# Optimization experiments

Hardware: AMD Instinct MI355X
Metric: run time of the kernel (lower is better)

## Reference

```python
import jax, jax.numpy as jnp
import numpy as np

NUM_EXECUTORS = 50
NUM_DAG_FEATURES = 3
EMB_DAG = 16
EMB_GLOB = 16
HIDDEN = [64, 64, 32]
B = 60000            # number of jobs (one per env in the batched rollout)
NODES_PER_JOB = 10
NODE_FEAT = 5


def _init_mlp(key, dims):
    ws, bs = [], []
    for i in range(len(dims) - 1):
        key, k = jax.random.split(key)
        scale = 1.0 / np.sqrt(dims[i])
        ws.append(jax.random.uniform(k, (dims[i], dims[i + 1]), jnp.float32, -scale, scale))
        bs.append(jnp.zeros((dims[i + 1],), jnp.float32))
    return ws, bs


def setup_inputs() -> dict:
    rng = np.random.default_rng(0)
    n_nodes = B * NODES_PER_JOB
    # dag_batch.ptr: job i owns nodes [i*NODES_PER_JOB, (i+1)*NODES_PER_JOB)
    ptr = np.arange(B + 1, dtype=np.int64) * NODES_PER_JOB
    job_indices = rng.permutation(B).astype(np.int64)
    # ragged action counts per job (exec_mask is a prefix mask of length num_exec_acts[i])
    num_exec_acts = rng.integers(1, NUM_EXECUTORS + 1, size=B).astype(np.int64)
    n_sel = num_exec_acts[job_indices]
    T = int(n_sel.sum())
    # per-ragged-row executor index: concat([arange(n) for n in n_sel]), vectorized
    starts = np.cumsum(n_sel) - n_sel
    exec_act_idx = (np.arange(T, dtype=np.int64) - np.repeat(starts, n_sel)).astype(np.int64)

    key = jax.random.key(0)
    k_x, k_hd, k_hg, k_mlp = jax.random.split(key, 4)
    x = jax.random.normal(k_x, (n_nodes, NODE_FEAT), jnp.float32)
    h_dag = jax.random.normal(k_hd, (B, EMB_DAG), jnp.float32)
    h_glob = jax.random.normal(k_hg, (B, EMB_GLOB), jnp.float32)

    in_dim = NUM_DAG_FEATURES + EMB_DAG + EMB_GLOB + 1  # 36
    ws, bs = _init_mlp(k_mlp, [in_dim] + HIDDEN + [1])

    return {
        "x": x,
        "h_dag": h_dag,
        "h_glob": h_glob,
        "ptr": jnp.asarray(ptr),
        "job_indices": jnp.asarray(job_indices),
        "num_exec_acts": jnp.asarray(num_exec_acts),
        "exec_act_idx": jnp.asarray(exec_act_idx),
        "W1": ws[0], "b1": bs[0],
        "W2": ws[1], "b2": bs[1],
        "W3": ws[2], "b3": bs[2],
        "W4": ws[3], "b4": bs[3],
    }


def reference(x, h_dag, h_glob, ptr, job_indices, num_exec_acts, exec_act_idx,
              W1, b1, W2, b2, W3, b3, W4, b4):
    T = exec_act_idx.shape[0]                       # total ragged action rows (static)
    J = job_indices.shape[0]
    # masked gather: dag features at each dag's start node, then select jobs
    x_dag = x[ptr[:-1], :NUM_DAG_FEATURES][job_indices]        # [J, 3]
    h_dag_sel = h_dag[job_indices]                              # [J, 16]
    x_h_dag = jnp.concatenate([x_dag, h_dag_sel], axis=1)       # [J, 19]
    # variable repeat_interleave -> gather by repeated row index
    n_sel = num_exec_acts[job_indices]
    rpt = jnp.repeat(jnp.arange(J), n_sel, total_repeat_length=T)
    x_h_rpt = x_h_dag[rpt]                                      # [T, 19]
    h_glob_rpt = h_glob[rpt]                                    # [T, 16]
    # exec action feature: k / num_executors for the k-th valid executor
    exec_actions = (exec_act_idx.astype(x.dtype) / NUM_EXECUTORS)[:, None]  # [T, 1]
    h = jnp.concatenate([x_h_rpt, h_glob_rpt, exec_actions], axis=1)        # [T, 36]
    h = jax.nn.relu(h @ W1 + b1)
    h = jax.nn.relu(h @ W2 + b2)
    h = jax.nn.relu(h @ W3 + b3)
    scores = (h @ W4 + b4).squeeze(-1)                          # [T]
    return scores
```

## Files before the change

kernel.cpp:

```cpp
#include <hip/hip_runtime.h>

#define TPB 256

using half8  = __attribute__((ext_vector_type(8))) _Float16;
using fp16x2 = __attribute__((ext_vector_type(2))) __fp16;
using f32x4  = __attribute__((ext_vector_type(4))) float;

static __device__ __forceinline__ unsigned short h2u(_Float16 h) {
    union { _Float16 h; unsigned short u; } v; v.h = h; return v.u;
}
static __device__ __forceinline__ unsigned pkrtz(float a, float b) {
    fp16x2 h = __builtin_amdgcn_cvt_pkrtz(a, b);
    return __builtin_bit_cast(unsigned, h);
}
template <int CTRL>
static __device__ __forceinline__ float dppmov(float x) {
    return __int_as_float(__builtin_amdgcn_mov_dpp(__float_as_int(x), CTRL, 0xF, 0xF, true));
}
#define DPP_SWAP 0xB1

__global__ __launch_bounds__(TPB) void k_prep(const float* __restrict__ x,
                                              const float* __restrict__ h_dag,
                                              const float* __restrict__ h_glob,
                                              const int* __restrict__ ptr,
                                              const int* __restrict__ job_indices,
                                              const int* __restrict__ num_exec_acts,
                                              int J, unsigned int* __restrict__ feat,
                                              int* __restrict__ bsum, int* __restrict__ jsv)
{
    __shared__ int sc[TPB];
    int j = blockIdx.x * TPB + threadIdx.x;
    int v = 0;
    if (j < J) {
        int ji   = job_indices[j];
        v        = num_exec_acts[ji];
        int node = ptr[ji];
        float f[40];
        f[0] = x[node * 5 + 0];
        f[1] = x[node * 5 + 1];
        f[2] = x[node * 5 + 2];
#pragma unroll
        for (int c = 0; c < 16; c++) f[3 + c]  = h_dag[ji * 16 + c];
#pragma unroll
        for (int c = 0; c < 16; c++) f[19 + c] = h_glob[j * 16 + c];
#pragma unroll
        for (int c = 35; c < 40; c++) f[c] = 0.0f;
        unsigned int w[20];
#pragma unroll
        for (int k = 0; k < 20; k++)
            w[k] = (unsigned)h2u((_Float16)f[2 * k]) | ((unsigned)h2u((_Float16)f[2 * k + 1]) << 16);
        uint4* dst = (uint4*)(feat + (size_t)j * 20);
#pragma unroll
        for (int qq = 0; qq < 5; qq++)
            dst[qq] = make_uint4(w[4 * qq], w[4 * qq + 1], w[4 * qq + 2], w[4 * qq + 3]);
    }
    sc[threadIdx.x] = v;
    __syncthreads();
    for (int d = 1; d < TPB; d <<= 1) {
        int add = (threadIdx.x >= d) ? sc[threadIdx.x - d] : 0;
        __syncthreads();
        sc[threadIdx.x] += add;
        __syncthreads();
    }
    if (j < J) jsv[j] = ((sc[threadIdx.x] - v) << 6) | v;
    if (threadIdx.x == TPB - 1) bsum[blockIdx.x] = sc[TPB - 1];
}

__global__ __launch_bounds__(TPB) void k_scan_wprep(const int* __restrict__ bsum, int nb,
                                                    int* __restrict__ boff,
                                                    const float* __restrict__ W1,
                                                    const float* __restrict__ b1,
                                                    const float* __restrict__ W2,
                                                    const float* __restrict__ b2,
                                                    const float* __restrict__ W3,
                                                    const float* __restrict__ b3,
                                                    const float* __restrict__ W4,
                                                    uint4* __restrict__ wfrag,
                                                    float4* __restrict__ bfrag)
{
    __shared__ int sc[TPB];
    int v = (threadIdx.x < nb) ? bsum[threadIdx.x] : 0;
    sc[threadIdx.x] = v;
    __syncthreads();
    for (int d = 1; d < TPB; d <<= 1) {
        int add = (threadIdx.x >= d) ? sc[threadIdx.x - d] : 0;
        __syncthreads();
        sc[threadIdx.x] += add;
        __syncthreads();
    }
    if (threadIdx.x < nb) boff[threadIdx.x] = sc[threadIdx.x] - v;

    if (threadIdx.x < 64) {
        int lane = threadIdx.x;
        int n = lane & 15, q = lane >> 4;
#pragma unroll
        for (int nt = 0; nt < 4; nt++) {
#pragma unroll
            for (int s = 0; s < 2; s++) {
                half8 w1f, w2f;
#pragma unroll
                for (int jj = 0; jj < 8; jj++) {
                    int ks = s * 32 + q * 8 + jj;
                    w1f[jj] = (ks < 36) ? (_Float16)W1[ks * 64 + nt * 16 + n] : (_Float16)0.0f;
                    w2f[jj] = (_Float16)W2[ks * 64 + nt * 16 + n];
                }
                wfrag[(nt * 2 + s) * 64 + lane]     = __builtin_bit_cast(uint4, w1f);
                wfrag[(8 + nt * 2 + s) * 64 + lane] = __builtin_bit_cast(uint4, w2f);
            }
        }
#pragma unroll
        for (int nt = 0; nt < 2; nt++) {
#pragma unroll
            for (int s = 0; s < 2; s++) {
                half8 w3f;
#pragma unroll
                for (int jj = 0; jj < 8; jj++) {
                    int ks = s * 32 + q * 8 + jj;
                    w3f[jj] = (_Float16)W3[ks * 32 + nt * 16 + n];
                }
                wfrag[(16 + nt * 2 + s) * 64 + lane] = __builtin_bit_cast(uint4, w3f);
            }
        }
        bfrag[0 * 64 + lane] = make_float4(b1[n], b1[16 + n], b1[32 + n], b1[48 + n]);
        bfrag[1 * 64 + lane] = make_float4(b2[n], b2[16 + n], b2[32 + n], b2[48 + n]);
        bfrag[2 * 64 + lane] = make_float4(b3[n], b3[16 + n], W4[n], W4[16 + n]);
    }
}

__global__ __launch_bounds__(TPB) void k_fill(const int* __restrict__ jsv,
                                              const int* __restrict__ boff,
                                              int J, int* __restrict__ rpt)
{
    int j = blockIdx.x * TPB + threadIdx.x;
    if (j >= J) return;
    int pv    = jsv[j];
    int v     = pv & 63;
    int start = boff[blockIdx.x] + (pv >> 6);
    for (int k = 0; k < v; k++) rpt[start + k] = j;
}

__global__ __launch_bounds__(TPB) void k_mlp_mfma(const unsigned int* __restrict__ feat,
                                                  const int* __restrict__ rpt,
                                                  const int* __restrict__ exec_act_idx,
                                                  const uint4* __restrict__ wfrag,
                                                  const float4* __restrict__ bfrag,
                                                  const float* __restrict__ b4,
                                                  float* __restrict__ out, int T, int numTiles)
{
    __shared__ __align__(16) char smem[4 * 8192];
    const int tid  = threadIdx.x;
    const int lane = tid & 63;
    const int wv   = tid >> 6;
    const int n    = lane & 15;
    const int q    = lane >> 4;
    char* slab0 = smem + wv * 8192;
    char* slab1 = slab0 + 4096;

    half8 bw1[4][2], bw2[4][2], bw3[2][2];
#pragma unroll
    for (int nt = 0; nt < 4; nt++)
#pragma unroll
        for (int s = 0; s < 2; s++) {
            bw1[nt][s] = __builtin_bit_cast(half8, wfrag[(nt * 2 + s) * 64 + lane]);
            bw2[nt][s] = __builtin_bit_cast(half8, wfrag[(8 + nt * 2 + s) * 64 + lane]);
        }
#pragma unroll
    for (int nt = 0; nt < 2; nt++)
#pragma unroll
        for (int s = 0; s < 2; s++)
            bw3[nt][s] = __builtin_bit_cast(half8, wfrag[(16 + nt * 2 + s) * 64 + lane]);

    float4 bf1 = bfrag[0 * 64 + lane];
    float4 bf2 = bfrag[1 * 64 + lane];
    float4 bf3 = bfrag[2 * 64 + lane];
    float bb1[4] = {bf1.x, bf1.y, bf1.z, bf1.w};
    float bb2[4] = {bf2.x, bf2.y, bf2.z, bf2.w};
    float bb3[2] = {bf3.x, bf3.y};
    const float w4a = bf3.z, w4b = bf3.w;
    const float b4v = b4[0];
    const int   swr = (n >> 1) & 7;
    const int   odd = n & 1;

    for (int tile = blockIdx.x; tile < numTiles; tile += gridDim.x) {
        const int rowbase = tile * 128 + wv * 32;

        half8 a1[2][2];
#pragma unroll
        for (int mt = 0; mt < 2; mt++) {
            int  rt    = rowbase + 16 * mt + n;
            bool valid = rt < T;
            int  j     = valid ? rpt[rt] : 0;
            const uint4* fsrc = (const uint4*)(feat + (size_t)j * 20);
            uint4 g0 = fsrc[q];
            a1[mt][0] = __builtin_bit_cast(half8, g0);
            uint4 g1 = make_uint4(0, 0, 0, 0);
            if (q == 0) {
                g1 = fsrc[4];
                float fe = valid ? (float)exec_act_idx[rt] * 0.02f : 0.0f;
                g1.y = (g1.y & 0xffffu) | ((unsigned)h2u((_Float16)fe) << 16);
            }
            a1[mt][1] = __builtin_bit_cast(half8, g1);
        }

#pragma unroll
        for (int mt = 0; mt < 2; mt++) {
            f32x4 acc[4];
#pragma unroll
            for (int nt = 0; nt < 4; nt++) { f32x4 c; c[0]=c[1]=c[2]=c[3]=bb1[nt]; acc[nt]=c; }
#pragma unroll
            for (int s = 0; s < 2; s++) {
#pragma unroll
                for (int nt = 0; nt < 4; nt++)
                    acc[nt] = __builtin_amdgcn_mfma_f32_16x16x32_f16(a1[mt][s], bw1[nt][s], acc[nt], 0, 0, 0);
            }
            unsigned* sl = (unsigned*)slab0;
#pragma unroll
            for (int nt = 0; nt < 4; nt++) {
                float v0 = fmaxf(acc[nt][0], 0.0f), v1 = fmaxf(acc[nt][1], 0.0f);
                float v2 = fmaxf(acc[nt][2], 0.0f), v3 = fmaxf(acc[nt][3], 0.0f);
                float t0 = dppmov<DPP_SWAP>(v0), t1 = dppmov<DPP_SWAP>(v1);
                float t2 = dppmov<DPP_SWAP>(v2), t3 = dppmov<DPP_SWAP>(v3);
                unsigned u0 = pkrtz(odd ? t2 : v0, odd ? v2 : t0);
                unsigned u1 = pkrtz(odd ? t3 : v1, odd ? v3 : t1);
                int rowA = 16 * mt + 4 * q + (odd ? 2 : 0);
                int c    = 2 * nt + (n >> 3);
                int a0   = (rowA * 8 + (c ^ ((rowA >> 1) & 7))) * 4 + ((n >> 1) & 3);
                sl[a0] = u0; sl[a0 + 32] = u1;
            }
        }

#pragma unroll
        for (int mt = 0; mt < 2; mt++) {
            const int M0 = 16 * mt;
            f32x4 acc[4];
#pragma unroll
            for (int nt = 0; nt < 4; nt++) { f32x4 c; c[0]=c[1]=c[2]=c[3]=bb2[nt]; acc[nt]=c; }
#pragma unroll
            for (int s = 0; s < 2; s++) {
                half8 a = *(const half8*)(slab0 + ((M0 + n) * 8 + ((s * 4 + q) ^ swr)) * 16);
#pragma unroll
                for (int nt = 0; nt < 4; nt++)
                    acc[nt] = __builtin_amdgcn_mfma_f32_16x16x32_f16(a, bw2[nt][s], acc[nt], 0, 0, 0);
            }
            unsigned* sl = (unsigned*)slab1;
#pragma unroll
            for (int nt = 0; nt < 4; nt++) {
                float v0 = fmaxf(acc[nt][0], 0.0f), v1 = fmaxf(acc[nt][1], 0.0f);
                float v2 = fmaxf(acc[nt][2], 0.0f), v3 = fmaxf(acc[nt][3], 0.0f);
                float t0 = dppmov<DPP_SWAP>(v0), t1 = dppmov<DPP_SWAP>(v1);
                float t2 = dppmov<DPP_SWAP>(v2), t3 = dppmov<DPP_SWAP>(v3);
                unsigned u0 = pkrtz(odd ? t2 : v0, odd ? v2 : t0);
                unsigned u1 = pkrtz(odd ? t3 : v1, odd ? v3 : t1);
                int rowA = M0 + 4 * q + (odd ? 2 : 0);
                int c    = 2 * nt + (n >> 3);
                int a0   = (rowA * 8 + (c ^ ((rowA >> 1) & 7))) * 4 + ((n >> 1) & 3);
                sl[a0] = u0; sl[a0 + 32] = u1;
            }
        }

#pragma unroll
        for (int mt = 0; mt < 2; mt++) {
            const int M0 = 16 * mt;
            f32x4 acc[2];
#pragma unroll
            for (int nt = 0; nt < 2; nt++) { f32x4 c; c[0]=c[1]=c[2]=c[3]=bb3[nt]; acc[nt]=c; }
#pragma unroll
            for (int s = 0; s < 2; s++) {
                half8 a = *(const half8*)(slab1 + ((M0 + n) * 8 + ((s * 4 + q) ^ swr)) * 16);
#pragma unroll
                for (int nt = 0; nt < 2; nt++)
                    acc[nt] = __builtin_amdgcn_mfma_f32_16x16x32_f16(a, bw3[nt][s], acc[nt], 0, 0, 0);
            }
            f32x4 red;
#pragma unroll
            for (int r = 0; r < 4; r++)
                red[r] = fmaxf(acc[0][r], 0.0f) * w4a + fmaxf(acc[1][r], 0.0f) * w4b;
#pragma unroll
            for (int r = 0; r < 4; r++) {
                red[r] += dppmov<0x121>(red[r]);
                red[r] += dppmov<0x122>(red[r]);
                red[r] += dppmov<0x124>(red[r]);
                red[r] += dppmov<0x128>(red[r]);
            }
            int t = rowbase + M0 + q * 4 + n;
            float val = (n == 0) ? red[0] : (n == 1) ? red[1] : (n == 2) ? red[2] : red[3];
            if (n < 4 && t < T) out[t] = val + b4v;
        }
    }
}

extern "C" void kernel_launch(void* const* d_in, const int* in_sizes, int n_in,
                              void* d_out, int out_size, void* d_ws, size_t ws_size,
                              hipStream_t stream)
{
    const float* x             = (const float*)d_in[0];
    const float* h_dag         = (const float*)d_in[1];
    const float* h_glob        = (const float*)d_in[2];
    const int*   ptr           = (const int*)d_in[3];
    const int*   job_indices   = (const int*)d_in[4];
    const int*   num_exec_acts = (const int*)d_in[5];
    const int*   exec_act_idx  = (const int*)d_in[6];
    const float* W1 = (const float*)d_in[7];
    const float* b1 = (const float*)d_in[8];
    const float* W2 = (const float*)d_in[9];
    const float* b2 = (const float*)d_in[10];
    const float* W3 = (const float*)d_in[11];
    const float* b3 = (const float*)d_in[12];
    const float* W4 = (const float*)d_in[13];
    const float* b4 = (const float*)d_in[14];
    float* out = (float*)d_out;

    int J  = in_sizes[4];
    int T  = in_sizes[6];
    int nb = (J + TPB - 1) / TPB;

    char* wsp = (char*)d_ws;
    int* rpt = (int*)wsp;
    wsp += (((size_t)T * 4) + 255) / 256 * 256;
    int* bsum = (int*)wsp;
    wsp += (((size_t)nb * 4) + 255) / 256 * 256;
    int* boff = (int*)wsp;
    wsp += (((size_t)nb * 4) + 255) / 256 * 256;
    int* jsv = (int*)wsp;
    wsp += (((size_t)J * 4) + 255) / 256 * 256;
    uint4* wfrag = (uint4*)wsp;
    wsp += 20 * 64 * 16;
    float4* bfrag = (float4*)wsp;
    wsp += 3 * 64 * 16;
    unsigned int* feat = (unsigned int*)wsp;

    k_prep<<<nb, TPB, 0, stream>>>(x, h_dag, h_glob, ptr, job_indices, num_exec_acts,
                                   J, feat, bsum, jsv);
    k_scan_wprep<<<1, TPB, 0, stream>>>(bsum, nb, boff, W1, b1, W2, b2, W3, b3, W4,
                                        wfrag, bfrag);
    k_fill<<<nb, TPB, 0, stream>>>(jsv, boff, J, rpt);

    int numTiles = (T + 127) / 128;
    int grid = numTiles < 1024 ? numTiles : 1024;
    k_mlp_mfma<<<grid, TPB, 0, stream>>>(feat, rpt, exec_act_idx, wfrag, bfrag, b4,
                                         out, T, numTiles);
}
```

Before: 183.6 us.

## Derive row-to-job map in MLP kernel, drop fill and scan kernels

```diff
diff --git a/kernel.cpp b/kernel.cpp
--- a/kernel.cpp
+++ b/kernel.cpp
@@ -25,9 +25,58 @@
                                               const int* __restrict__ ptr,
                                               const int* __restrict__ job_indices,
                                               const int* __restrict__ num_exec_acts,
-                                              int J, unsigned int* __restrict__ feat,
-                                              int* __restrict__ bsum, int* __restrict__ jsv)
+                                              int J, int nb,
+                                              unsigned int* __restrict__ feat,
+                                              int* __restrict__ bsum, int* __restrict__ jsv,
+                                              const float* __restrict__ W1,
+                                              const float* __restrict__ b1,
+                                              const float* __restrict__ W2,
+                                              const float* __restrict__ b2,
+                                              const float* __restrict__ W3,
+                                              const float* __restrict__ b3,
+                                              const float* __restrict__ W4,
+                                              uint4* __restrict__ wfrag,
+                                              float4* __restrict__ bfrag)
 {
+    if (blockIdx.x == (unsigned)nb) {
+        if (threadIdx.x < 64) {
+            int lane = threadIdx.x;
+            int n = lane & 15, q = lane >> 4;
+#pragma unroll
+            for (int nt = 0; nt < 4; nt++) {
+#pragma unroll
+                for (int s = 0; s < 2; s++) {
+                    half8 w1f, w2f;
+#pragma unroll
+                    for (int jj = 0; jj < 8; jj++) {
+                        int ks = s * 32 + q * 8 + jj;
+                        w1f[jj] = (ks < 36) ? (_Float16)W1[ks * 64 + nt * 16 + n] : (_Float16)0.0f;
+                        w2f[jj] = (_Float16)W2[ks * 64 + nt * 16 + n];
+                    }
+                    wfrag[(nt * 2 + s) * 64 + lane]     = __builtin_bit_cast(uint4, w1f);
+                    wfrag[(8 + nt * 2 + s) * 64 + lane] = __builtin_bit_cast(uint4, w2f);
+                }
+            }
+#pragma unroll
+            for (int nt = 0; nt < 2; nt++) {
+#pragma unroll
+                for (int s = 0; s < 2; s++) {
+                    half8 w3f;
+#pragma unroll
+                    for (int jj = 0; jj < 8; jj++) {
+                        int ks = s * 32 + q * 8 + jj;
+                        w3f[jj] = (_Float16)W3[ks * 32 + nt * 16 + n];
+                    }
+                    wfrag[(16 + nt * 2 + s) * 64 + lane] = __builtin_bit_cast(uint4, w3f);
+                }
+            }
+            bfrag[0 * 64 + lane] = make_float4(b1[n], b1[16 + n], b1[32 + n], b1[48 + n]);
+            bfrag[1 * 64 + lane] = make_float4(b2[n], b2[16 + n], b2[32 + n], b2[48 + n]);
+            bfrag[2 * 64 + lane] = make_float4(b3[n], b3[16 + n], W4[n], W4[16 + n]);
+        }
+        return;
+    }
+
     __shared__ int sc[TPB];
     int j = blockIdx.x * TPB + threadIdx.x;
     int v = 0;
@@ -66,95 +115,40 @@
     if (threadIdx.x == TPB - 1) bsum[blockIdx.x] = sc[TPB - 1];
 }
 
-__global__ __launch_bounds__(TPB) void k_scan_wprep(const int* __restrict__ bsum, int nb,
-                                                    int* __restrict__ boff,
-                                                    const float* __restrict__ W1,
-                                                    const float* __restrict__ b1,
-                                                    const float* __restrict__ W2,
-                                                    const float* __restrict__ b2,
-                                                    const float* __restrict__ W3,
-                                                    const float* __restrict__ b3,
-                                                    const float* __restrict__ W4,
-                                                    uint4* __restrict__ wfrag,
-                                                    float4* __restrict__ bfrag)
+__global__ __launch_bounds__(TPB, 5) void k_mlp_mfma(const unsigned int* __restrict__ feat,
+                                                     const int* __restrict__ jsv,
+                                                     const int* __restrict__ bsum,
+                                                     const uint4* __restrict__ wfrag,
+                                                     const float4* __restrict__ bfrag,
+                                                     const float* __restrict__ b4,
+                                                     float* __restrict__ out,
+                                                     int T, int J, int nb, int numTiles, int chunk)
 {
-    __shared__ int sc[TPB];
-    int v = (threadIdx.x < nb) ? bsum[threadIdx.x] : 0;
-    sc[threadIdx.x] = v;
-    __syncthreads();
-    for (int d = 1; d < TPB; d <<= 1) {
-        int add = (threadIdx.x >= d) ? sc[threadIdx.x - d] : 0;
-        __syncthreads();
-        sc[threadIdx.x] += add;
-        __syncthreads();
-    }
-    if (threadIdx.x < nb) boff[threadIdx.x] = sc[threadIdx.x] - v;
-
-    if (threadIdx.x < 64) {
-        int lane = threadIdx.x;
-        int n = lane & 15, q = lane >> 4;
-#pragma unroll
-        for (int nt = 0; nt < 4; nt++) {
-#pragma unroll
-            for (int s = 0; s < 2; s++) {
-                half8 w1f, w2f;
-#pragma unroll
-                for (int jj = 0; jj < 8; jj++) {
-                    int ks = s * 32 + q * 8 + jj;
-                    w1f[jj] = (ks < 36) ? (_Float16)W1[ks * 64 + nt * 16 + n] : (_Float16)0.0f;
-                    w2f[jj] = (_Float16)W2[ks * 64 + nt * 16 + n];
-                }
-                wfrag[(nt * 2 + s) * 64 + lane]     = __builtin_bit_cast(uint4, w1f);
-                wfrag[(8 + nt * 2 + s) * 64 + lane] = __builtin_bit_cast(uint4, w2f);
-            }
-        }
-#pragma unroll
-        for (int nt = 0; nt < 2; nt++) {
-#pragma unroll
-            for (int s = 0; s < 2; s++) {
-                half8 w3f;
-#pragma unroll
-                for (int jj = 0; jj < 8; jj++) {
-                    int ks = s * 32 + q * 8 + jj;
-                    w3f[jj] = (_Float16)W3[ks * 32 + nt * 16 + n];
-                }
-                wfrag[(16 + nt * 2 + s) * 64 + lane] = __builtin_bit_cast(uint4, w3f);
-            }
-        }
-        bfrag[0 * 64 + lane] = make_float4(b1[n], b1[16 + n], b1[32 + n], b1[48 + n]);
-        bfrag[1 * 64 + lane] = make_float4(b2[n], b2[16 + n], b2[32 + n], b2[48 + n]);
-        bfrag[2 * 64 + lane] = make_float4(b3[n], b3[16 + n], W4[n], W4[16 + n]);
-    }
-}
-
-__global__ __launch_bounds__(TPB) void k_fill(const int* __restrict__ jsv,
-                                              const int* __restrict__ boff,
-                                              int J, int* __restrict__ rpt)
-{
-    int j = blockIdx.x * TPB + threadIdx.x;
-    if (j >= J) return;
-    int pv    = jsv[j];
-    int v     = pv & 63;
-    int start = boff[blockIdx.x] + (pv >> 6);
-    for (int k = 0; k < v; k++) rpt[start + k] = j;
-}
-
-__global__ __launch_bounds__(TPB) void k_mlp_mfma(const unsigned int* __restrict__ feat,
-                                                  const int* __restrict__ rpt,
-                                                  const int* __restrict__ exec_act_idx,
-                                                  const uint4* __restrict__ wfrag,
-                                                  const float4* __restrict__ bfrag,
-                                                  const float* __restrict__ b4,
-                                                  float* __restrict__ out, int T, int numTiles)
-{
-    __shared__ __align__(16) char smem[4 * 8192];
+    __shared__ __align__(16) char smem[4 * 4096];
+    __shared__ int boffs[TPB];
+    __shared__ int swin[4][64];
     const int tid  = threadIdx.x;
     const int lane = tid & 63;
     const int wv   = tid >> 6;
     const int n    = lane & 15;
     const int q    = lane >> 4;
-    char* slab0 = smem + wv * 8192;
-    char* slab1 = slab0 + 4096;
+    char* slab = smem + wv * 4096;
+
+    {
+        int v = (tid < nb) ? bsum[tid] : 0;
+        boffs[tid] = v;
+        __syncthreads();
+        for (int d = 1; d < TPB; d <<= 1) {
+            int add = (tid >= d) ? boffs[tid - d] : 0;
+            __syncthreads();
+            boffs[tid] += add;
+            __syncthreads();
+        }
+        int ex = boffs[tid] - v;
+        __syncthreads();
+        boffs[tid] = ex;
+        __syncthreads();
+    }
 
     half8 bw1[4][2], bw2[4][2], bw3[2][2];
 #pragma unroll
@@ -181,22 +175,58 @@
     const int   swr = (n >> 1) & 7;
     const int   odd = n & 1;
 
-    for (int tile = blockIdx.x; tile < numTiles; tile += gridDim.x) {
+    const int t0 = blockIdx.x * chunk;
+    const int t1 = (t0 + chunk < numTiles) ? (t0 + chunk) : numTiles;
+
+    int j_lo;
+    {
+        int r0 = t0 * 128 + wv * 32;
+        int lo = 0, hi = nb - 1;
+        while (lo < hi) {
+            int mid = (lo + hi + 1) >> 1;
+            if (boffs[mid] <= r0) lo = mid; else hi = mid - 1;
+        }
+        j_lo = lo << 8;
+    }
+
+    for (int tile = t0; tile < t1; ++tile) {
         const int rowbase = tile * 128 + wv * 32;
+
+        for (;;) {
+            int jj = j_lo + lane;
+            int s  = (jj < J) ? (boffs[jj >> 8] + (jsv[jj] >> 6)) : 0x7fffffff;
+            unsigned long long m = __ballot(s <= rowbase);
+            if (m == ~0ULL) { j_lo += 63; continue; }
+            j_lo += 63 - __builtin_clzll(m);
+            break;
+        }
+        {
+            int jj = j_lo + lane;
+            int s  = (jj < J) ? (boffs[jj >> 8] + (jsv[jj] >> 6)) : 0x7fffffff;
+            swin[wv][lane] = s;
+        }
 
         half8 a1[2][2];
 #pragma unroll
         for (int mt = 0; mt < 2; mt++) {
             int  rt    = rowbase + 16 * mt + n;
             bool valid = rt < T;
-            int  j     = valid ? rpt[rt] : 0;
+            int l = 0;
+#pragma unroll
+            for (int stp = 32; stp; stp >>= 1) {
+                int cand = l + stp;
+                if (cand < 64 && swin[wv][cand] <= rt) l = cand;
+            }
+            int j     = j_lo + l;
+            if (j > J - 1) j = J - 1;
+            int start = swin[wv][l];
             const uint4* fsrc = (const uint4*)(feat + (size_t)j * 20);
             uint4 g0 = fsrc[q];
             a1[mt][0] = __builtin_bit_cast(half8, g0);
             uint4 g1 = make_uint4(0, 0, 0, 0);
             if (q == 0) {
                 g1 = fsrc[4];
-                float fe = valid ? (float)exec_act_idx[rt] * 0.02f : 0.0f;
+                float fe = valid ? (float)(rt - start) * 0.02f : 0.0f;
                 g1.y = (g1.y & 0xffffu) | ((unsigned)h2u((_Float16)fe) << 16);
             }
             a1[mt][1] = __builtin_bit_cast(half8, g1);
@@ -213,15 +243,15 @@
                 for (int nt = 0; nt < 4; nt++)
                     acc[nt] = __builtin_amdgcn_mfma_f32_16x16x32_f16(a1[mt][s], bw1[nt][s], acc[nt], 0, 0, 0);
             }
-            unsigned* sl = (unsigned*)slab0;
+            unsigned* sl = (unsigned*)slab;
 #pragma unroll
             for (int nt = 0; nt < 4; nt++) {
                 float v0 = fmaxf(acc[nt][0], 0.0f), v1 = fmaxf(acc[nt][1], 0.0f);
                 float v2 = fmaxf(acc[nt][2], 0.0f), v3 = fmaxf(acc[nt][3], 0.0f);
-                float t0 = dppmov<DPP_SWAP>(v0), t1 = dppmov<DPP_SWAP>(v1);
-                float t2 = dppmov<DPP_SWAP>(v2), t3 = dppmov<DPP_SWAP>(v3);
-                unsigned u0 = pkrtz(odd ? t2 : v0, odd ? v2 : t0);
-                unsigned u1 = pkrtz(odd ? t3 : v1, odd ? v3 : t1);
+                float t0_ = dppmov<DPP_SWAP>(v0), t1_ = dppmov<DPP_SWAP>(v1);
+                float t2_ = dppmov<DPP_SWAP>(v2), t3_ = dppmov<DPP_SWAP>(v3);
+                unsigned u0 = pkrtz(odd ? t2_ : v0, odd ? v2 : t0_);
+                unsigned u1 = pkrtz(odd ? t3_ : v1, odd ? v3 : t1_);
                 int rowA = 16 * mt + 4 * q + (odd ? 2 : 0);
                 int c    = 2 * nt + (n >> 3);
                 int a0   = (rowA * 8 + (c ^ ((rowA >> 1) & 7))) * 4 + ((n >> 1) & 3);
@@ -237,20 +267,20 @@
             for (int nt = 0; nt < 4; nt++) { f32x4 c; c[0]=c[1]=c[2]=c[3]=bb2[nt]; acc[nt]=c; }
 #pragma unroll
             for (int s = 0; s < 2; s++) {
-                half8 a = *(const half8*)(slab0 + ((M0 + n) * 8 + ((s * 4 + q) ^ swr)) * 16);
+                half8 a = *(const half8*)(slab + ((M0 + n) * 8 + ((s * 4 + q) ^ swr)) * 16);
 #pragma unroll
                 for (int nt = 0; nt < 4; nt++)
                     acc[nt] = __builtin_amdgcn_mfma_f32_16x16x32_f16(a, bw2[nt][s], acc[nt], 0, 0, 0);
             }
-            unsigned* sl = (unsigned*)slab1;
+            unsigned* sl = (unsigned*)slab;
 #pragma unroll
             for (int nt = 0; nt < 4; nt++) {
                 float v0 = fmaxf(acc[nt][0], 0.0f), v1 = fmaxf(acc[nt][1], 0.0f);
                 float v2 = fmaxf(acc[nt][2], 0.0f), v3 = fmaxf(acc[nt][3], 0.0f);
-                float t0 = dppmov<DPP_SWAP>(v0), t1 = dppmov<DPP_SWAP>(v1);
-                float t2 = dppmov<DPP_SWAP>(v2), t3 = dppmov<DPP_SWAP>(v3);
-                unsigned u0 = pkrtz(odd ? t2 : v0, odd ? v2 : t0);
-                unsigned u1 = pkrtz(odd ? t3 : v1, odd ? v3 : t1);
+                float t0_ = dppmov<DPP_SWAP>(v0), t1_ = dppmov<DPP_SWAP>(v1);
+                float t2_ = dppmov<DPP_SWAP>(v2), t3_ = dppmov<DPP_SWAP>(v3);
+                unsigned u0 = pkrtz(odd ? t2_ : v0, odd ? v2 : t0_);
+                unsigned u1 = pkrtz(odd ? t3_ : v1, odd ? v3 : t1_);
                 int rowA = M0 + 4 * q + (odd ? 2 : 0);
                 int c    = 2 * nt + (n >> 3);
                 int a0   = (rowA * 8 + (c ^ ((rowA >> 1) & 7))) * 4 + ((n >> 1) & 3);
@@ -266,7 +296,7 @@
             for (int nt = 0; nt < 2; nt++) { f32x4 c; c[0]=c[1]=c[2]=c[3]=bb3[nt]; acc[nt]=c; }
 #pragma unroll
             for (int s = 0; s < 2; s++) {
-                half8 a = *(const half8*)(slab1 + ((M0 + n) * 8 + ((s * 4 + q) ^ swr)) * 16);
+                half8 a = *(const half8*)(slab + ((M0 + n) * 8 + ((s * 4 + q) ^ swr)) * 16);
 #pragma unroll
                 for (int nt = 0; nt < 2; nt++)
                     acc[nt] = __builtin_amdgcn_mfma_f32_16x16x32_f16(a, bw3[nt][s], acc[nt], 0, 0, 0);
@@ -299,7 +329,6 @@
     const int*   ptr           = (const int*)d_in[3];
     const int*   job_indices   = (const int*)d_in[4];
     const int*   num_exec_acts = (const int*)d_in[5];
-    const int*   exec_act_idx  = (const int*)d_in[6];
     const float* W1 = (const float*)d_in[7];
     const float* b1 = (const float*)d_in[8];
     const float* W2 = (const float*)d_in[9];
@@ -315,11 +344,7 @@
     int nb = (J + TPB - 1) / TPB;
 
     char* wsp = (char*)d_ws;
-    int* rpt = (int*)wsp;
-    wsp += (((size_t)T * 4) + 255) / 256 * 256;
     int* bsum = (int*)wsp;
-    wsp += (((size_t)nb * 4) + 255) / 256 * 256;
-    int* boff = (int*)wsp;
     wsp += (((size_t)nb * 4) + 255) / 256 * 256;
     int* jsv = (int*)wsp;
     wsp += (((size_t)J * 4) + 255) / 256 * 256;
@@ -329,14 +354,14 @@
     wsp += 3 * 64 * 16;
     unsigned int* feat = (unsigned int*)wsp;
 
-    k_prep<<<nb, TPB, 0, stream>>>(x, h_dag, h_glob, ptr, job_indices, num_exec_acts,
-                                   J, feat, bsum, jsv);
-    k_scan_wprep<<<1, TPB, 0, stream>>>(bsum, nb, boff, W1, b1, W2, b2, W3, b3, W4,
-                                        wfrag, bfrag);
-    k_fill<<<nb, TPB, 0, stream>>>(jsv, boff, J, rpt);
+    k_prep<<<nb + 1, TPB, 0, stream>>>(x, h_dag, h_glob, ptr, job_indices, num_exec_acts,
+                                       J, nb, feat, bsum, jsv,
+                                       W1, b1, W2, b2, W3, b3, W4, wfrag, bfrag);
 
     int numTiles = (T + 127) / 128;
-    int grid = numTiles < 1024 ? numTiles : 1024;
-    k_mlp_mfma<<<grid, TPB, 0, stream>>>(feat, rpt, exec_act_idx, wfrag, bfrag, b4,
-                                         out, T, numTiles);
-}
+    int grid = numTiles < 1280 ? numTiles : 1280;
+    int chunk = (numTiles + grid - 1) / grid;
+    grid = (numTiles + chunk - 1) / chunk;
+    k_mlp_mfma<<<grid, TPB, 0, stream>>>(feat, jsv, bsum, wfrag, bfrag, b4,
+                                         out, T, J, nb, numTiles, chunk);
+}
```

Measured after the change: 351.9 us. 1.92x slower.
